# Optimization experiments

Measured on AMD Instinct MI355X. Metric: run time of the kernel, lower is better.

## Reference

```python
import jax, jax.numpy as jnp
import numpy as np

N, E, D = 50000, 640000, 128


def setup_inputs() -> dict:
    key = jax.random.key(0)
    ks = jax.random.split(key, 10)
    scale = (2.0 / (D + D)) ** 0.5  # xavier-ish scale for square weights

    def w(k):
        return jax.random.normal(k, (D, D), jnp.float32) * scale

    return {
        "x": jax.random.normal(ks[0], (N, D), jnp.float32),
        "view2": jax.random.normal(ks[1], (N, D), jnp.float32),
        "W_neigh1": w(ks[2]),
        "W_self1": w(ks[3]),
        "b_self1": jnp.zeros((D,), jnp.float32),
        "W_neigh2": w(ks[4]),
        "W_self2": w(ks[5]),
        "b_self2": jnp.zeros((D,), jnp.float32),
        "W_attn": w(ks[6]),
        "b_attn": jnp.zeros((D,), jnp.float32),
        "att": jax.random.normal(ks[7], (1, D), jnp.float32) * 0.1,
        "src": jax.random.randint(ks[8], (E,), 0, N),
        "dst": jax.random.randint(ks[9], (E,), 0, N),
    }


def _sage_mean(h, src, dst, W_neigh, W_self, b_self, n):
    """DGL SAGEConv, aggregator_type='mean', in_feats==out_feats (lin after mp)."""
    msgs = h[src]  # gather: [E, D]
    s = jax.ops.segment_sum(msgs, dst, num_segments=n)  # scatter-add: [N, D]
    deg = jax.ops.segment_sum(jnp.ones((src.shape[0],), h.dtype), dst, num_segments=n)
    h_neigh = jnp.where(deg[:, None] > 0, s / jnp.maximum(deg, 1.0)[:, None], 0.0)
    # rst = fc_self(h_self) + fc_neigh(h_neigh)
    return h @ W_self.T + b_self + h_neigh @ W_neigh.T


def reference(x, view2, W_neigh1, W_self1, b_self1, W_neigh2, W_self2, b_self2,
              W_attn, b_attn, att, src, dst):
    n = x.shape[0]
    # SAGENet: outs = [h, l1(h)/1, l2(l1(h))/2]; res = sum(outs)
    h1 = _sage_mean(x, src, dst, W_neigh1, W_self1, b_self1, n)
    h2 = _sage_mean(h1, src, dst, W_neigh2, W_self2, b_self2, n)
    res = x + h1 + h2 * 0.5
    # Attn semantic fusion over embedding views [res, view2]
    embeds = (res, view2)
    scores = jnp.stack(
        [att[0] @ jnp.tanh(e @ W_attn.T + b_attn).mean(axis=0) for e in embeds]
    )  # [2]
    beta = jax.nn.softmax(scores)
    return beta[0] * res + beta[1] * view2
```

## Files before the change

kernel.cpp:

```cpp
#include <hip/hip_runtime.h>

#define DD 128

using bf16 = __bf16;
typedef __bf16 bf16x8 __attribute__((ext_vector_type(8)));
typedef float f32x4 __attribute__((ext_vector_type(4)));
typedef float f32x2 __attribute__((ext_vector_type(2)));

__device__ inline bf16x8 cvt8(const float* p) {
  f32x4 v0 = *(const f32x4*)p;
  f32x4 v1 = *(const f32x4*)(p + 4);
  bf16x8 r;
  r[0] = (bf16)v0[0]; r[1] = (bf16)v0[1]; r[2] = (bf16)v0[2]; r[3] = (bf16)v0[3];
  r[4] = (bf16)v1[0]; r[5] = (bf16)v1[1]; r[6] = (bf16)v1[2]; r[7] = (bf16)v1[3];
  return r;
}

__device__ inline uint2 pk8fp8(const float* f) {
  int u0 = __builtin_amdgcn_cvt_pk_fp8_f32(f[0], f[1], 0, 0);
  u0 = __builtin_amdgcn_cvt_pk_fp8_f32(f[2], f[3], u0, 1);
  int u1 = __builtin_amdgcn_cvt_pk_fp8_f32(f[4], f[5], 0, 0);
  u1 = __builtin_amdgcn_cvt_pk_fp8_f32(f[6], f[7], u1, 1);
  uint2 r; r.x = (unsigned)u0; r.y = (unsigned)u1; return r;
}

__device__ inline void acc4fp8(unsigned w, float* a) {
  f32x2 p;
  p = __builtin_amdgcn_cvt_pk_f32_fp8(w, 0); a[0] += p.x; a[1] += p.y;
  p = __builtin_amdgcn_cvt_pk_f32_fp8(w, 1); a[2] += p.x; a[3] += p.y;
}

__device__ inline float ftanh(float x) {
  float e2 = __expf(2.0f * x);
  return 1.0f - 2.0f * __builtin_amdgcn_rcpf(e2 + 1.0f);
}

__device__ inline int swz(int o) { return o ^ (((o >> 8) & 7) << 4); }

__global__ void k_prep(int* __restrict__ cnt, int N,
                       const float* __restrict__ w0, const float* __restrict__ w1,
                       const float* __restrict__ w2, const float* __restrict__ w3,
                       const float* __restrict__ w4, bf16* __restrict__ wb, int totalW,
                       const float* __restrict__ x, bf16* __restrict__ xb,
                       unsigned char* __restrict__ xb8, int total8,
                       int nbZ, int nbW) {
  int b = blockIdx.x;
  if (b < nbZ) {
    int i = b * 256 + threadIdx.x;
    if (i < N) cnt[i] = 0;
  } else if (b < nbZ + nbW) {
    int i = (b - nbZ) * 256 + threadIdx.x;
    if (i < totalW) {
      int m = i >> 14;
      int r = i & 16383;
      const float* s = m == 0 ? w0 : m == 1 ? w1 : m == 2 ? w2 : m == 3 ? w3 : w4;
      wb[i] = (bf16)s[r];
    }
  } else {
    int i = (b - nbZ - nbW) * 256 + threadIdx.x;
    if (i < total8) {
      float f[8];
      f32x4 v0 = *(const f32x4*)(x + (size_t)i * 8);
      f32x4 v1 = *(const f32x4*)(x + (size_t)i * 8 + 4);
#pragma unroll
      for (int j = 0; j < 4; ++j) { f[j] = v0[j]; f[4 + j] = v1[j]; }
      bf16x8 r;
#pragma unroll
      for (int j = 0; j < 8; ++j) r[j] = (bf16)f[j];
      *(bf16x8*)(xb + (size_t)i * 8) = r;
      *(uint2*)(xb8 + (size_t)i * 8) = pk8fp8(f);
    }
  }
}

__global__ void k_cvt8(const bf16* __restrict__ h, unsigned char* __restrict__ h8,
                       int total8) {
  int i = blockIdx.x * 256 + threadIdx.x;
  if (i >= total8) return;
  bf16x8 v = *(const bf16x8*)(h + (size_t)i * 8);
  float f[8];
#pragma unroll
  for (int j = 0; j < 8; ++j) f[j] = (float)v[j];
  *(uint2*)(h8 + (size_t)i * 8) = pk8fp8(f);
}

__global__ void k_hist(const int* __restrict__ dst, int* __restrict__ cnt, int E) {
  int e = blockIdx.x * 256 + threadIdx.x;
  if (e < E) atomicAdd(&cnt[dst[e]], 1);
}

__global__ __launch_bounds__(256) void k_scan1(const int* __restrict__ cnt,
                                               int* __restrict__ bsum, int N) {
  __shared__ int sm[256];
  int t = threadIdx.x;
  int i = blockIdx.x * 256 + t;
  sm[t] = (i < N) ? cnt[i] : 0;
  __syncthreads();
#pragma unroll
  for (int d = 128; d > 0; d >>= 1) {
    if (t < d) sm[t] += sm[t + d];
    __syncthreads();
  }
  if (t == 0) bsum[blockIdx.x] = sm[0];
}

__global__ __launch_bounds__(256) void k_scan2(int* __restrict__ bsum, int nb) {
  __shared__ int sm[256];
  int t = threadIdx.x;
  int v = (t < nb) ? bsum[t] : 0;
  sm[t] = v;
  __syncthreads();
#pragma unroll
  for (int d = 1; d < 256; d <<= 1) {
    int u = (t >= d) ? sm[t - d] : 0;
    __syncthreads();
    sm[t] += u;
    __syncthreads();
  }
  if (t < nb) bsum[t] = sm[t] - v;
}

__global__ __launch_bounds__(256) void k_scan3(const int* __restrict__ cnt,
                                               const int* __restrict__ bsum,
                                               int* __restrict__ offs,
                                               int* __restrict__ cursor, int N) {
  __shared__ int sm[256];
  int t = threadIdx.x;
  int i = blockIdx.x * 256 + t;
  int v = (i < N) ? cnt[i] : 0;
  sm[t] = v;
  __syncthreads();
#pragma unroll
  for (int d = 1; d < 256; d <<= 1) {
    int u = (t >= d) ? sm[t - d] : 0;
    __syncthreads();
    sm[t] += u;
    __syncthreads();
  }
  int incl = sm[t];
  int base = bsum[blockIdx.x];
  if (i < N) {
    int ex = base + incl - v;
    offs[i] = ex;
    cursor[i] = ex;
    if (i == N - 1) offs[N] = base + incl;
  }
}

__global__ void k_scatter(const int* __restrict__ src, const int* __restrict__ dst,
                          int* __restrict__ cursor, int* __restrict__ ssrc, int E) {
  int e = blockIdx.x * 256 + threadIdx.x;
  if (e < E) {
    int d = dst[e];
    int p = atomicAdd(&cursor[d], 1);
    ssrc[p] = src[e];
  }
}

template <int MODE>
__global__ __launch_bounds__(1024, 1) void k_layer(const bf16* __restrict__ Hb,
                                                   const unsigned char* __restrict__ Hb8,
                                                   const int* __restrict__ offs,
                                                   const int* __restrict__ ssrc,
                                                   const bf16* __restrict__ Wsb,
                                                   const bf16* __restrict__ Wnb,
                                                   const float* __restrict__ bias,
                                                   const float* __restrict__ Xres,
                                                   bf16* __restrict__ H1out,
                                                   bf16* __restrict__ Resb, int N) {
  __shared__ char smem[65536];
  int t = threadIdx.x;
#pragma unroll
  for (int m = 0; m < 2; ++m) {
    const bf16* wsrc = m ? Wnb : Wsb;
#pragma unroll
    for (int it = 0; it < 2; ++it) {
      int o = (it * 1024 + t) * 16;
      *(bf16x8*)(smem + m * 32768 + swz(o)) = *(const bf16x8*)(wsrc + o / 2);
    }
  }
  __syncthreads();

  int wv = t >> 6;
  int lane = t & 63;
  int tile = wv * gridDim.x + blockIdx.x;
  int n0 = tile << 4;
  if (n0 >= N) return;
  int lr = lane & 15;
  int g = lane >> 4;

  int node = n0 + lr;

  const bf16* a1p = Hb + (size_t)node * DD + g * 32;
  bf16x8 a1[4];
#pragma unroll
  for (int kk = 0; kk < 4; ++kk) a1[kk] = *(const bf16x8*)(a1p + kk * 8);

  int beg = offs[node], end = offs[node + 1];
  float acc[4][8];
#pragma unroll
  for (int kk = 0; kk < 4; ++kk)
#pragma unroll
    for (int j = 0; j < 8; ++j) acc[kk][j] = 0.f;
  for (int i = beg; i < end; ++i) {
    int s = ssrc[i];
    const unsigned char* hp = Hb8 + (size_t)s * DD + g * 32;
    uint4 u0 = *(const uint4*)(hp);
    uint4 u1 = *(const uint4*)(hp + 16);
    acc4fp8(u0.x, &acc[0][0]); acc4fp8(u0.y, &acc[0][4]);
    acc4fp8(u0.z, &acc[1][0]); acc4fp8(u0.w, &acc[1][4]);
    acc4fp8(u1.x, &acc[2][0]); acc4fp8(u1.y, &acc[2][4]);
    acc4fp8(u1.z, &acc[3][0]); acc4fp8(u1.w, &acc[3][4]);
  }
  float inv = (end > beg) ? 1.0f / (float)(end - beg) : 0.f;
  bf16x8 a2[4];
#pragma unroll
  for (int kk = 0; kk < 4; ++kk)
#pragma unroll
    for (int j = 0; j < 8; ++j) a2[kk][j] = (bf16)(acc[kk][j] * inv);

  int rb = n0 + (g << 2);
#pragma unroll
  for (int j = 0; j < 8; ++j) {
    int row = j * 16 + lr;
    int rbase = row * 256 + g * 64;
    f32x4 cs = {0.f, 0.f, 0.f, 0.f};
    f32x4 cn = {0.f, 0.f, 0.f, 0.f};
#pragma unroll
    for (int kk = 0; kk < 4; ++kk) {
      int ro = swz(rbase + kk * 16);
      bf16x8 bs = *(const bf16x8*)(smem + ro);
      bf16x8 bn = *(const bf16x8*)(smem + 32768 + ro);
      cs = __builtin_amdgcn_mfma_f32_16x16x32_bf16(a1[kk], bs, cs, 0, 0, 0);
      cn = __builtin_amdgcn_mfma_f32_16x16x32_bf16(a2[kk], bn, cn, 0, 0, 0);
    }
    int col = j * 16 + lr;
    float bb = bias[col];
#pragma unroll
    for (int r = 0; r < 4; ++r) {
      size_t idx = (size_t)(rb + r) * DD + col;
      float v = cs[r] + cn[r] + bb;
      if (MODE == 0) H1out[idx] = (bf16)v;
      else           Resb[idx] = (bf16)(Xres[idx] + (float)Hb[idx] + 0.5f * v);
    }
  }
}

__global__ __launch_bounds__(512, 4) void k_attn2(const bf16* __restrict__ resb,
                                                  const float* __restrict__ v2f,
                                                  const bf16* __restrict__ Wab,
                                                  const float* __restrict__ bias,
                                                  const float* __restrict__ att,
                                                  float* __restrict__ partial,
                                                  int nbA, int N) {
  __shared__ char smem[32768];
  __shared__ float smr[8];
  int t = threadIdx.x;
#pragma unroll
  for (int it = 0; it < 4; ++it) {
    int o = (it * 512 + t) * 16;
    *(bf16x8*)(smem + swz(o)) = *(const bf16x8*)(Wab + o / 2);
  }
  __syncthreads();

  int wv = t >> 6;
  int lane = t & 63;
  int gwid = blockIdx.x * 8 + wv;
  int view = gwid & 1;
  int tile = gwid >> 1;
  int n0 = tile << 4;
  float part = 0.f;
  if (n0 < N) {
    int lr = lane & 15;
    int lk = (lane >> 4) << 3;
    bf16x8 a[4];
    if (view) {
      const float* ap = v2f + (size_t)(n0 + lr) * DD + lk;
#pragma unroll
      for (int kk = 0; kk < 4; ++kk) a[kk] = cvt8(ap + kk * 32);
    } else {
      const bf16* ap = resb + (size_t)(n0 + lr) * DD + lk;
#pragma unroll
      for (int kk = 0; kk < 4; ++kk) a[kk] = *(const bf16x8*)(ap + kk * 32);
    }
#pragma unroll
    for (int j = 0; j < 8; ++j) {
      int row = j * 16 + lr;
      int rbase = row * 256 + lk * 2;
      f32x4 c = {0.f, 0.f, 0.f, 0.f};
#pragma unroll
      for (int kk = 0; kk < 4; ++kk) {
        bf16x8 bw = *(const bf16x8*)(smem + swz(rbase + kk * 64));
        c = __builtin_amdgcn_mfma_f32_16x16x32_bf16(a[kk], bw, c, 0, 0, 0);
      }
      int col = j * 16 + lr;
      float aw = att[col], bb = bias[col];
#pragma unroll
      for (int r = 0; r < 4; ++r) part += aw * ftanh(c[r] + bb);
    }
  }
#pragma unroll
  for (int d = 1; d < 64; d <<= 1) part += __shfl_xor(part, d);
  if (lane == 0) smr[wv] = part;
  __syncthreads();
  if (t == 0) {
    partial[blockIdx.x]       = smr[0] + smr[2] + smr[4] + smr[6];
    partial[nbA + blockIdx.x] = smr[1] + smr[3] + smr[5] + smr[7];
  }
}

__global__ __launch_bounds__(256) void k_score(const float* __restrict__ partial,
                                               float* __restrict__ scores, int nbA) {
  __shared__ float sm[256];
  int t = threadIdx.x;
#pragma unroll
  for (int v = 0; v < 2; ++v) {
    float s = 0.f;
    for (int i = t; i < nbA; i += 256) s += partial[v * nbA + i];
    sm[t] = s;
    __syncthreads();
#pragma unroll
    for (int d = 128; d > 0; d >>= 1) {
      if (t < d) sm[t] += sm[t + d];
      __syncthreads();
    }
    if (t == 0) scores[v] = sm[0];
    __syncthreads();
  }
}

__global__ void k_fin(float* __restrict__ out, const bf16* __restrict__ resb,
                      const float* __restrict__ v2,
                      const float* __restrict__ scores, float invN, int total8) {
  int i = blockIdx.x * 256 + threadIdx.x;
  if (i >= total8) return;
  float s0 = scores[0] * invN, s1 = scores[1] * invN;
  float m = fmaxf(s0, s1);
  float e0 = expf(s0 - m), e1 = expf(s1 - m);
  float inv = 1.0f / (e0 + e1);
  float b0 = e0 * inv, b1 = e1 * inv;
  bf16x8 r = ((const bf16x8*)resb)[i];
  f32x4 w0 = ((const f32x4*)v2)[2 * i];
  f32x4 w1 = ((const f32x4*)v2)[2 * i + 1];
  f32x4 o0, o1;
#pragma unroll
  for (int j = 0; j < 4; ++j) {
    o0[j] = b0 * (float)r[j] + b1 * w0[j];
    o1[j] = b0 * (float)r[4 + j] + b1 * w1[j];
  }
  ((f32x4*)out)[2 * i] = o0;
  ((f32x4*)out)[2 * i + 1] = o1;
}

extern "C" void kernel_launch(void* const* d_in, const int* in_sizes, int n_in,
                              void* d_out, int out_size, void* d_ws, size_t ws_size,
                              hipStream_t stream) {
  const float* x   = (const float*)d_in[0];
  const float* v2  = (const float*)d_in[1];
  const float* Wn1 = (const float*)d_in[2];
  const float* Ws1 = (const float*)d_in[3];
  const float* b1  = (const float*)d_in[4];
  const float* Wn2 = (const float*)d_in[5];
  const float* Ws2 = (const float*)d_in[6];
  const float* b2  = (const float*)d_in[7];
  const float* Wa  = (const float*)d_in[8];
  const float* ba  = (const float*)d_in[9];
  const float* att = (const float*)d_in[10];
  const int*  src  = (const int*)d_in[11];
  const int*  dst  = (const int*)d_in[12];
  const int D = in_sizes[4];
  const int N = in_sizes[0] / D;
  const int E = in_sizes[11];
  float* out = (float*)d_out;

  char* ws = (char*)d_ws;
  size_t o = 0;
  auto alloc = [&](size_t bytes) -> void* {
    void* p = ws + o;
    o += (bytes + 255) & ~(size_t)255;
    return p;
  };
  int*  cnt    = (int*)alloc((size_t)N * 4);
  int*  offs   = (int*)alloc((size_t)(N + 1) * 4);
  int*  cursor = (int*)alloc((size_t)N * 4);
  int*  ssrc   = (int*)alloc((size_t)E * 4);
  bf16* xb     = (bf16*)alloc((size_t)N * D * 2);
  bf16* h1b    = (bf16*)alloc((size_t)N * D * 2);
  bf16* resb   = (bf16*)alloc((size_t)N * D * 2);
  unsigned char* xb8  = (unsigned char*)alloc((size_t)N * D);
  unsigned char* h1b8 = (unsigned char*)alloc((size_t)N * D);
  bf16* wb     = (bf16*)alloc((size_t)5 * D * D * 2);
  float* sc    = (float*)alloc(2 * 4);
  int nb = (N + 255) / 256;
  int*  bsum   = (int*)alloc((size_t)nb * 4);

  int tilesPerView = (N + 15) / 16;
  int attnWaves = 2 * tilesPerView;
  int nbA = (attnWaves + 7) / 8;
  float* apart = (float*)alloc((size_t)2 * nbA * 4);

  int nbZ = (N + 255) / 256;
  int nbW = (5 * D * D + 255) / 256;
  int nbX = (N * D / 8 + 255) / 256;
  k_prep<<<nbZ + nbW + nbX, 256, 0, stream>>>(cnt, N, Ws1, Wn1, Ws2, Wn2, Wa, wb,
                                              5 * D * D, x, xb, xb8, N * D / 8,
                                              nbZ, nbW);

  k_hist<<<(E + 255) / 256, 256, 0, stream>>>(dst, cnt, E);
  k_scan1<<<nb, 256, 0, stream>>>(cnt, bsum, N);
  k_scan2<<<1, 256, 0, stream>>>(bsum, nb);
  k_scan3<<<nb, 256, 0, stream>>>(cnt, bsum, offs, cursor, N);
  k_scatter<<<(E + 255) / 256, 256, 0, stream>>>(src, dst, cursor, ssrc, E);

  int layerBlocks = 256;

  k_layer<0><<<layerBlocks, 1024, 0, stream>>>(xb, xb8, offs, ssrc, wb, wb + D * D,
                                               b1, nullptr, h1b, nullptr, N);
  k_cvt8<<<(N * D / 8 + 255) / 256, 256, 0, stream>>>(h1b, h1b8, N * D / 8);
  k_layer<1><<<layerBlocks, 1024, 0, stream>>>(h1b, h1b8, offs, ssrc, wb + 2 * D * D,
                                               wb + 3 * D * D, b2, x, nullptr, resb, N);
  k_attn2<<<nbA, 512, 0, stream>>>(resb, v2, wb + 4 * D * D, ba, att, apart, nbA, N);
  k_score<<<1, 256, 0, stream>>>(apart, sc, nbA);
  k_fin<<<((N * D / 8) + 255) / 256, 256, 0, stream>>>(out, resb, v2, sc,
                                                       1.0f / (float)N, N * D / 8);
}
```

Measured before the change: 170.5 us.

## Partition histogram and scatter atomics by destination range per XCD

The histogram and CSR scatter kernels now use a fixed grid of 2048 blocks. Each group of blocks, selected by blockIdx mod 8, handles only destinations in one eighth of the node range, using a grid-stride loop over all edges. The aim is to keep the atomics for a given destination slice on one XCD's L2, avoiding cross-die contention and coherence traffic. In exchange, every partition rereads the whole dst array, which multiplies index read traffic by eight. It also relies on blocks being dispatched round-robin across XCDs.

```diff
diff --git a/kernel.cpp b/kernel.cpp
--- a/kernel.cpp
+++ b/kernel.cpp
@@ -84,9 +84,34 @@
   *(uint2*)(h8 + (size_t)i * 8) = pk8fp8(f);
 }
 
-__global__ void k_hist(const int* __restrict__ dst, int* __restrict__ cnt, int E) {
-  int e = blockIdx.x * 256 + threadIdx.x;
-  if (e < E) atomicAdd(&cnt[dst[e]], 1);
+__global__ void k_hist(const int* __restrict__ dst, int* __restrict__ cnt,
+                       int E, int N) {
+  int p = blockIdx.x & 7;
+  int slice = blockIdx.x >> 3;
+  int nslice = gridDim.x >> 3;
+  int lo = p * (N >> 3);
+  int hi = (p == 7) ? N : lo + (N >> 3);
+  for (int e = slice * 256 + threadIdx.x; e < E; e += nslice * 256) {
+    int d = dst[e];
+    if (d >= lo && d < hi) atomicAdd(&cnt[d], 1);
+  }
+}
+
+__global__ void k_scatter(const int* __restrict__ src, const int* __restrict__ dst,
+                          int* __restrict__ cursor, int* __restrict__ ssrc,
+                          int E, int N) {
+  int p = blockIdx.x & 7;
+  int slice = blockIdx.x >> 3;
+  int nslice = gridDim.x >> 3;
+  int lo = p * (N >> 3);
+  int hi = (p == 7) ? N : lo + (N >> 3);
+  for (int e = slice * 256 + threadIdx.x; e < E; e += nslice * 256) {
+    int d = dst[e];
+    if (d >= lo && d < hi) {
+      int pos = atomicAdd(&cursor[d], 1);
+      ssrc[pos] = src[e];
+    }
+  }
 }
 
 __global__ __launch_bounds__(256) void k_scan1(const int* __restrict__ cnt,
@@ -144,16 +169,6 @@
     offs[i] = ex;
     cursor[i] = ex;
     if (i == N - 1) offs[N] = base + incl;
-  }
-}
-
-__global__ void k_scatter(const int* __restrict__ src, const int* __restrict__ dst,
-                          int* __restrict__ cursor, int* __restrict__ ssrc, int E) {
-  int e = blockIdx.x * 256 + threadIdx.x;
-  if (e < E) {
-    int d = dst[e];
-    int p = atomicAdd(&cursor[d], 1);
-    ssrc[p] = src[e];
   }
 }
 
@@ -406,11 +421,11 @@
                                               5 * D * D, x, xb, xb8, N * D / 8,
                                               nbZ, nbW);
 
-  k_hist<<<(E + 255) / 256, 256, 0, stream>>>(dst, cnt, E);
+  k_hist<<<2048, 256, 0, stream>>>(dst, cnt, E, N);
   k_scan1<<<nb, 256, 0, stream>>>(cnt, bsum, N);
   k_scan2<<<1, 256, 0, stream>>>(bsum, nb);
   k_scan3<<<nb, 256, 0, stream>>>(cnt, bsum, offs, cursor, N);
-  k_scatter<<<(E + 255) / 256, 256, 0, stream>>>(src, dst, cursor, ssrc, E);
+  k_scatter<<<2048, 256, 0, stream>>>(src, dst, cursor, ssrc, E, N);
 
   int layerBlocks = 256;
 
```

Measured after the change: 166.9 us. -2.1%, faster.
